# Optimization experiments

Hardware: AMD Instinct MI355X
Metric: run time of the kernel (lower is better)

The kernel has to match this reference:

```python
import jax, jax.numpy as jnp
import numpy as np

B, S, D, DIM = 8, 4096, 1024, 512  # batch, src nodes, dst nodes, feature dim


def setup_inputs() -> dict:
    key = jax.random.key(0)
    k1, k2, k3, k4, k5 = jax.random.split(key, 5)
    scale = 1.0 / np.sqrt(DIM)
    return {
        "src_val": jax.random.normal(k1, (B, S, DIM), dtype=jnp.float32),
        "src_state": jax.random.normal(k2, (B, S), dtype=jnp.float32),
        "dst_val": jax.random.normal(k3, (B, D, DIM), dtype=jnp.float32),
        "W_route": jax.random.normal(k4, (DIM, DIM), dtype=jnp.float32) * scale,
        "W_val": jax.random.normal(k5, (DIM, DIM), dtype=jnp.float32) * scale,
    }


def reference(src_val, src_state, dst_val, W_route, W_val):
    # Pairwise route logits: bilinear bipartite attention, [B, S, D]
    inv_sqrt_d = 1.0 / jnp.sqrt(jnp.asarray(src_val.shape[-1], src_val.dtype))
    q = jnp.einsum("bsd,de->bse", src_val, W_route)
    logits = jnp.einsum("bse,bke->bsk", q, dst_val) * inv_sqrt_d
    # route compression: softmax over dst nodes (dim=-1)
    routes = jax.nn.softmax(logits, axis=-1)
    # projections
    projected_val = jnp.einsum("bsd,de->bse", src_val, W_val)  # [B, S, DIM]
    projected_state = src_state                                 # identity state proj, [B, S]
    sender_strength = jax.nn.softplus(src_state)                # [B, S]
    # weighted routing + accumulation
    weighted_routes = routes * sender_strength[..., None]       # [B, S, D]
    delta_state = jnp.einsum("bsk,bs->bk", weighted_routes, projected_state)   # [B, D]
    delta_val = jnp.einsum("bsk,bsd->bkd", weighted_routes, projected_val)     # [B, D, DIM]
    return delta_state, delta_val
```

## Files before the change

### kernel.cpp

```cpp
#include <hip/hip_runtime.h>
#include <hip/hip_fp16.h>

#define B_   8
#define S_   4096
#define DD_  1024
#define DIM_ 512
#define SCALE 0.044194173824159216f

typedef __bf16 bf16x8 __attribute__((ext_vector_type(8)));
typedef float  floatx4 __attribute__((ext_vector_type(4)));

__device__ inline unsigned short f2bf(float f) {
    union { float f; unsigned int u; } v; v.f = f;
    unsigned int r = v.u + 0x7fffu + ((v.u >> 16) & 1u);
    return (unsigned short)(r >> 16);
}
__device__ inline float bf2f(unsigned short h) {
    union { unsigned int u; float f; } v; v.u = ((unsigned int)h) << 16;
    return v.f;
}
__device__ inline uint4 cvt8(const float* __restrict__ g) {
    float4 f0 = *(const float4*)g;
    float4 f1 = *(const float4*)(g + 4);
    unsigned short tmp[8] = {f2bf(f0.x), f2bf(f0.y), f2bf(f0.z), f2bf(f0.w),
                             f2bf(f1.x), f2bf(f1.y), f2bf(f1.z), f2bf(f1.w)};
    return *(const uint4*)tmp;
}
__device__ inline void async16(unsigned short* lds, const unsigned short* g) {
    __builtin_amdgcn_global_load_lds(
        (const __attribute__((address_space(1))) void*)g,
        (__attribute__((address_space(3))) void*)lds, 16, 0, 0);
}

template <int AF32, int BF32>
__device__ inline void mainloop(unsigned short* As, unsigned short* Bs,
                                const void* Ap, size_t lda,
                                const void* Bp, size_t ldb,
                                int kIters, floatx4 (&acc)[4][4]) {
    const int t = threadIdx.x, lane = t & 63, wave = t >> 6;
    const int rA = t >> 2, cA = (t & 3) * 8;
    const int mrow = (wave >> 1) * 64, ncol = (wave & 1) * 64;
    const int fr = lane & 15, fk = (lane >> 4) * 8;

    const unsigned short* gA16 = nullptr; const float* gA32 = nullptr;
    const unsigned short* gB16 = nullptr; const float* gB32 = nullptr;
    if (AF32) gA32 = (const float*)Ap + (size_t)rA * lda + cA;
    else      gA16 = (const unsigned short*)Ap + (size_t)rA * lda + cA;
    if (BF32) gB32 = (const float*)Bp + (size_t)rA * ldb + cA;
    else      gB16 = (const unsigned short*)Bp + (size_t)rA * ldb + cA;

    unsigned short* ldsA = As + wave * 512;
    unsigned short* ldsB = Bs + wave * 512;

    for (int kt = 0; kt < kIters; ++kt) {
        if (AF32) {
            *(uint4*)&As[t * 8]        = cvt8(gA32);
            *(uint4*)&As[2048 + t * 8] = cvt8(gA32 + 64 * lda);
            gA32 += 32;
        } else {
            async16(ldsA,        gA16);
            async16(ldsA + 2048, gA16 + 64 * lda);
            gA16 += 32;
        }
        if (BF32) {
            *(uint4*)&Bs[t * 8]        = cvt8(gB32);
            *(uint4*)&Bs[2048 + t * 8] = cvt8(gB32 + 64 * ldb);
            gB32 += 32;
        } else {
            async16(ldsB,        gB16);
            async16(ldsB + 2048, gB16 + 64 * ldb);
            gB16 += 32;
        }
        __syncthreads();
        bf16x8 af[4], bfr[4];
#pragma unroll
        for (int i = 0; i < 4; ++i)
            af[i] = *(const bf16x8*)&As[(mrow + i * 16 + fr) * 32 + fk];
#pragma unroll
        for (int j = 0; j < 4; ++j)
            bfr[j] = *(const bf16x8*)&Bs[(ncol + j * 16 + fr) * 32 + fk];
#pragma unroll
        for (int i = 0; i < 4; ++i)
#pragma unroll
            for (int j = 0; j < 4; ++j)
                acc[i][j] = __builtin_amdgcn_mfma_f32_16x16x32_bf16(af[i], bfr[j],
                                                                    acc[i][j], 0, 0, 0);
        __syncthreads();
    }
}

#define EPILOGUE_COORDS                                     \
    const int lane = threadIdx.x & 63, wave = threadIdx.x >> 6; \
    const int mrow = (wave >> 1) * 64, ncol = (wave & 1) * 64;  \
    const int col = lane & 15, q = lane >> 4;

#define ACC_INIT                                            \
    floatx4 acc[4][4];                                      \
    _Pragma("unroll") for (int i = 0; i < 4; ++i)           \
        _Pragma("unroll") for (int j = 0; j < 4; ++j)       \
            acc[i][j] = (floatx4){0.f, 0.f, 0.f, 0.f};

__global__ __launch_bounds__(256) void k_prep(const float* __restrict__ src,
                                              unsigned short* __restrict__ srcb,
                                              const float* __restrict__ dst,
                                              unsigned short* __restrict__ dstb) {
    const int t = threadIdx.x;
    if (blockIdx.x < 8192) {
        const size_t idx = ((size_t)blockIdx.x * 256 + t) * 8;
        *(uint4*)&srcb[idx] = cvt8(src + idx);
    } else {
        const size_t idx = ((size_t)(blockIdx.x - 8192) * 256 + t) * 8;
        *(uint4*)&dstb[idx] = cvt8(dst + idx);
    }
}

__global__ __launch_bounds__(256) void k_dstWr(const unsigned short* __restrict__ dstb,
                                               const float* __restrict__ Wr,
                                               unsigned short* __restrict__ DW) {
    __shared__ unsigned short As[128 * 32];
    __shared__ unsigned short Bs[128 * 32];
    const int n0 = blockIdx.x * 128, m0 = blockIdx.y * 128;
    ACC_INIT
    mainloop<0, 1>(As, Bs, dstb + (size_t)m0 * DIM_, DIM_,
                   Wr + (size_t)n0 * DIM_, DIM_, DIM_ / 32, acc);
    EPILOGUE_COORDS
#pragma unroll
    for (int i = 0; i < 4; ++i)
#pragma unroll
        for (int j = 0; j < 4; ++j)
#pragma unroll
            for (int r = 0; r < 4; ++r)
                DW[(size_t)(m0 + mrow + i * 16 + q * 4 + r) * DIM_ +
                   n0 + ncol + j * 16 + col] = f2bf(acc[i][j][r] * SCALE);
}

__global__ __launch_bounds__(256) void k_logitsT(const unsigned short* __restrict__ DW,
                                                 const unsigned short* __restrict__ srcb,
                                                 unsigned short* __restrict__ LTb,
                                                 float* __restrict__ Lpart) {
    __shared__ unsigned short As[128 * 32];
    __shared__ unsigned short Bs[128 * 32];
    __shared__ float csum[8][128];
    const int n = blockIdx.x;
    const int b = n & 7;
    const int rem = n >> 3;
    const int xs = rem >> 3;
    const int yd = rem & 7;
    const int n0 = xs * 128, m0 = yd * 128;
    ACC_INIT
    mainloop<0, 0>(As, Bs,
                   DW + (size_t)b * DD_ * DIM_ + (size_t)m0 * DIM_, DIM_,
                   srcb + (size_t)b * S_ * DIM_ + (size_t)n0 * DIM_, DIM_,
                   DIM_ / 32, acc);
    EPILOGUE_COORDS
    unsigned short* LT = LTb + (size_t)b * DD_ * S_;
    float psum[4] = {0.f, 0.f, 0.f, 0.f};
#pragma unroll
    for (int i = 0; i < 4; ++i)
#pragma unroll
        for (int j = 0; j < 4; ++j)
#pragma unroll
            for (int r = 0; r < 4; ++r) {
                float e = __expf(acc[i][j][r]);
                LT[(size_t)(m0 + mrow + i * 16 + q * 4 + r) * S_ +
                   n0 + ncol + j * 16 + col] = f2bf(e);
                psum[j] += e;
            }
    const int slice = (wave >> 1) * 4 + q;
#pragma unroll
    for (int j = 0; j < 4; ++j) csum[slice][ncol + j * 16 + col] = psum[j];
    __syncthreads();
    const int t = threadIdx.x;
    if (t < 128) {
        float v = 0.f;
#pragma unroll
        for (int k = 0; k < 8; ++k) v += csum[k][t];
        Lpart[((size_t)b * 8 + yd) * S_ + n0 + t] = v;
    }
}

__global__ __launch_bounds__(256) void k_finalize(const float* __restrict__ state,
                                                  const float* __restrict__ Lpart,
                                                  float* __restrict__ scale) {
    const int i = blockIdx.x * 256 + threadIdx.x;
    const int b = i >> 12, s = i & (S_ - 1);
    float d = 0.f;
#pragma unroll
    for (int k = 0; k < 8; ++k) d += Lpart[((size_t)b * 8 + k) * S_ + s];
    const float st = state[i];
    const float sp = (st > 15.f) ? st : log1pf(__expf(st));
    scale[i] = sp / d;
}

__global__ __launch_bounds__(256) void k_srcT(const unsigned short* __restrict__ srcb,
                                              const float* __restrict__ scale,
                                              unsigned short* __restrict__ srcST) {
    __shared__ unsigned short Ts[64 * 65];
    const int s0 = blockIdx.x * 64, d0 = blockIdx.y * 64, b = blockIdx.z;
    const int t = threadIdx.x;
    {
        const int r = t >> 2, c0 = (t & 3) * 16;
        const unsigned short* g =
            srcb + (size_t)b * S_ * DIM_ + (size_t)(s0 + r) * DIM_ + d0 + c0;
        uint4 v0 = *(const uint4*)g;
        uint4 v1 = *(const uint4*)(g + 8);
        const unsigned short* e0 = (const unsigned short*)&v0;
        const unsigned short* e1 = (const unsigned short*)&v1;
        const float sc = scale[(size_t)b * S_ + s0 + r];
#pragma unroll
        for (int i = 0; i < 8; ++i) {
            Ts[r * 65 + c0 + i]     = f2bf(bf2f(e0[i]) * sc);
            Ts[r * 65 + c0 + 8 + i] = f2bf(bf2f(e1[i]) * sc);
        }
    }
    __syncthreads();
    {
        const int rr = t >> 2, c0 = (t & 3) * 16;
        unsigned short tmp[16];
#pragma unroll
        for (int j = 0; j < 16; ++j) tmp[j] = Ts[(c0 + j) * 65 + rr];
        unsigned short* o =
            srcST + (size_t)b * DIM_ * S_ + (size_t)(d0 + rr) * S_ + s0 + c0;
        *(uint4*)o = *(const uint4*)tmp;
        *(uint4*)(o + 8) = *(const uint4*)(tmp + 8);
    }
}

__global__ __launch_bounds__(256) void k_dstate(const unsigned short* __restrict__ LT,
                                                const float* __restrict__ state,
                                                const float* __restrict__ scale,
                                                float* __restrict__ out) {
    const int b = blockIdx.y;
    const int dd = blockIdx.x * 4 + (threadIdx.x >> 6);
    const int lane = threadIdx.x & 63;
    const unsigned short* row = LT + (size_t)b * DD_ * S_ + (size_t)dd * S_;
    const float* st = state + (size_t)b * S_;
    const float* sc = scale + (size_t)b * S_;

    float acc = 0.f;
#pragma unroll
    for (int it = 0; it < S_ / 512; ++it) {
        const int s = it * 512 + lane * 8;
        uint4 v = *(const uint4*)(row + s);
        const unsigned short* e = (const unsigned short*)&v;
        float4 f0 = *(const float4*)(st + s);
        float4 f1 = *(const float4*)(st + s + 4);
        float4 c0 = *(const float4*)(sc + s);
        float4 c1 = *(const float4*)(sc + s + 4);
        acc += bf2f(e[0]) * f0.x * c0.x + bf2f(e[1]) * f0.y * c0.y +
               bf2f(e[2]) * f0.z * c0.z + bf2f(e[3]) * f0.w * c0.w +
               bf2f(e[4]) * f1.x * c1.x + bf2f(e[5]) * f1.y * c1.y +
               bf2f(e[6]) * f1.z * c1.z + bf2f(e[7]) * f1.w * c1.w;
    }
#pragma unroll
    for (int off = 32; off; off >>= 1) acc += __shfl_down(acc, off);
    if (lane == 0) out[(size_t)b * DD_ + dd] = acc;
}

__global__ __launch_bounds__(256) void k_dU(const unsigned short* __restrict__ LTb,
                                            const unsigned short* __restrict__ srcST,
                                            __half* __restrict__ Pp) {
    __shared__ unsigned short As[128 * 32];
    __shared__ unsigned short Bs[128 * 32];
    const int n = blockIdx.x;
    const int z = (n & 7) + 8 * (n >> 8);
    const int rem = (n >> 3) & 31;
    const int xe = rem >> 3;
    const int yd = rem & 7;
    const int b = z >> 2, ks = z & 3;
    const int n0 = xe * 128, m0 = yd * 128;
    ACC_INIT
    mainloop<0, 0>(As, Bs,
                   LTb + (size_t)b * DD_ * S_ + (size_t)m0 * S_ + ks * 1024, S_,
                   srcST + (size_t)b * DIM_ * S_ + (size_t)n0 * S_ + ks * 1024, S_,
                   1024 / 32, acc);
    EPILOGUE_COORDS
    __half* O = Pp + (size_t)ks * B_ * DD_ * DIM_ + (size_t)b * DD_ * DIM_;
#pragma unroll
    for (int i = 0; i < 4; ++i)
#pragma unroll
        for (int j = 0; j < 4; ++j)
#pragma unroll
            for (int r = 0; r < 4; ++r)
                O[(size_t)(m0 + mrow + i * 16 + q * 4 + r) * DIM_ +
                  n0 + ncol + j * 16 + col] = __float2half(acc[i][j][r]);
}

__global__ __launch_bounds__(256) void k_reduceU(const __half* __restrict__ Pp,
                                                 unsigned short* __restrict__ U,
                                                 const float* __restrict__ Wv,
                                                 unsigned short* __restrict__ WvT) {
    __shared__ float Ts[64 * 68];
    const int t = threadIdx.x;
    if (blockIdx.x < 2048) {
        const size_t idx = ((size_t)blockIdx.x * 256 + t) * 8;
        const size_t n = (size_t)B_ * DD_ * DIM_;
        float o[8] = {0.f, 0.f, 0.f, 0.f, 0.f, 0.f, 0.f, 0.f};
#pragma unroll
        for (int ks = 0; ks < 4; ++ks) {
            uint4 v = *(const uint4*)(Pp + (size_t)ks * n + idx);
            const __half* h = (const __half*)&v;
#pragma unroll
            for (int j = 0; j < 8; ++j) o[j] += __half2float(h[j]);
        }
        unsigned short tmp[8];
#pragma unroll
        for (int j = 0; j < 8; ++j) tmp[j] = f2bf(o[j]);
        *(uint4*)&U[idx] = *(const uint4*)tmp;
        return;
    }
    const int n2 = blockIdx.x - 2048;
    const int d0 = (n2 & 7) * 64, e0 = (n2 >> 3) * 64;
    {
        const int r = t >> 2, c0 = (t & 3) * 16;
        const float* g = Wv + (size_t)(d0 + r) * DIM_ + e0 + c0;
#pragma unroll
        for (int i = 0; i < 4; ++i)
            *(float4*)&Ts[r * 68 + c0 + i * 4] = *(const float4*)(g + i * 4);
    }
    __syncthreads();
    {
        const int rr = t >> 2, c0 = (t & 3) * 16;
        unsigned short tmp[16];
#pragma unroll
        for (int j = 0; j < 16; ++j) tmp[j] = f2bf(Ts[(c0 + j) * 68 + rr]);
        unsigned short* o = WvT + (size_t)(e0 + rr) * DIM_ + d0 + c0;
        *(uint4*)o = *(const uint4*)tmp;
        *(uint4*)(o + 8) = *(const uint4*)(tmp + 8);
    }
}

__global__ __launch_bounds__(256) void k_dvalW(const unsigned short* __restrict__ U,
                                               const unsigned short* __restrict__ WvT,
                                               float* __restrict__ d_val) {
    __shared__ unsigned short As[128 * 32];
    __shared__ unsigned short Bs[128 * 32];
    const int n0 = blockIdx.x * 128, m0 = blockIdx.y * 128;
    ACC_INIT
    mainloop<0, 0>(As, Bs, U + (size_t)m0 * DIM_, DIM_,
                   WvT + (size_t)n0 * DIM_, DIM_, DIM_ / 32, acc);
    EPILOGUE_COORDS
#pragma unroll
    for (int i = 0; i < 4; ++i)
#pragma unroll
        for (int j = 0; j < 4; ++j)
#pragma unroll
            for (int r = 0; r < 4; ++r)
                d_val[(size_t)(m0 + mrow + i * 16 + q * 4 + r) * DIM_ +
                      n0 + ncol + j * 16 + col] = acc[i][j][r];
}

extern "C" void kernel_launch(void* const* d_in, const int* in_sizes, int n_in,
                              void* d_out, int out_size, void* d_ws, size_t ws_size,
                              hipStream_t stream) {
    const float* src   = (const float*)d_in[0];
    const float* state = (const float*)d_in[1];
    const float* dst   = (const float*)d_in[2];
    const float* Wr    = (const float*)d_in[3];
    const float* Wv    = (const float*)d_in[4];

    unsigned short* srcb = (unsigned short*)d_ws;
    __half* Pp = (__half*)d_ws;
    unsigned short* LT = srcb + (size_t)B_ * S_ * DIM_;
    unsigned short* U  = LT;
    unsigned short* WvT = U + (size_t)B_ * DD_ * DIM_;
    unsigned short* C = LT + (size_t)B_ * DD_ * S_;
    unsigned short* dstb = C;
    unsigned short* DW = dstb + (size_t)B_ * DD_ * DIM_;
    float* Lpart = (float*)(DW + (size_t)B_ * DD_ * DIM_);
    unsigned short* srcST = C;

    float* d_state = (float*)d_out;
    float* d_val   = (float*)d_out + B_ * DD_;
    float* scale   = d_val;

    k_prep<<<dim3(8192 + 2048), 256, 0, stream>>>(src, srcb, dst, dstb);
    k_dstWr<<<dim3(DIM_ / 128, (B_ * DD_) / 128), 256, 0, stream>>>(dstb, Wr, DW);
    k_logitsT<<<dim3(2048), 256, 0, stream>>>(DW, srcb, LT, Lpart);
    k_finalize<<<dim3((B_ * S_) / 256), 256, 0, stream>>>(state, Lpart, scale);
    k_dstate<<<dim3(DD_ / 4, B_), 256, 0, stream>>>(LT, state, scale, d_state);
    k_srcT<<<dim3(S_ / 64, DIM_ / 64, B_), 256, 0, stream>>>(srcb, scale, srcST);
    k_dU<<<dim3(1024), 256, 0, stream>>>(LT, srcST, Pp);
    k_reduceU<<<dim3(2048 + 64), 256, 0, stream>>>(Pp, U, Wv, WvT);
    k_dvalW<<<dim3(DIM_ / 128, (B_ * DD_) / 128), 256, 0, stream>>>(U, WvT, d_val);
}
```

Baseline: 298.0 us.

## Fold delta_state into dU GEMM and stage epilogue stores through LDS

Removes the separate k_dstate kernel, which re-read the whole exp-logit matrix LT. Instead, the xe==0 blocks of k_dU compute a dot product of the LT tile already in LDS with precomputed scale*state weights, and k_reduceU sums the per-split partials. The epilogues of k_logitsT and k_dU now go through an LDS staging buffer, replacing scattered 2-byte global stores with coalesced 16-byte row writes. This costs extra LDS, more barriers, and some load imbalance on the folding blocks.

Measured after the change: 314.9 us. 5.7% more time.

```diff
diff --git a/kernel.cpp b/kernel.cpp
--- a/kernel.cpp
+++ b/kernel.cpp
@@ -18,6 +18,10 @@
 __device__ inline float bf2f(unsigned short h) {
     union { unsigned int u; float f; } v; v.u = ((unsigned int)h) << 16;
     return v.f;
+}
+__device__ inline unsigned short f2h(float f) {
+    __half h = __float2half(f);
+    union { __half h; unsigned short u; } v; v.h = h; return v.u;
 }
 __device__ inline uint4 cvt8(const float* __restrict__ g) {
     float4 f0 = *(const float4*)g;
@@ -140,6 +144,7 @@
                                                  float* __restrict__ Lpart) {
     __shared__ unsigned short As[128 * 32];
     __shared__ unsigned short Bs[128 * 32];
+    __shared__ __align__(16) unsigned short Rep[64 * 136];
     __shared__ float csum[8][128];
     const int n = blockIdx.x;
     const int b = n & 7;
@@ -153,24 +158,55 @@
                    srcb + (size_t)b * S_ * DIM_ + (size_t)n0 * DIM_, DIM_,
                    DIM_ / 32, acc);
     EPILOGUE_COORDS
+    const int t = threadIdx.x;
     unsigned short* LT = LTb + (size_t)b * DD_ * S_;
     float psum[4] = {0.f, 0.f, 0.f, 0.f};
-#pragma unroll
-    for (int i = 0; i < 4; ++i)
-#pragma unroll
-        for (int j = 0; j < 4; ++j)
-#pragma unroll
-            for (int r = 0; r < 4; ++r) {
-                float e = __expf(acc[i][j][r]);
-                LT[(size_t)(m0 + mrow + i * 16 + q * 4 + r) * S_ +
-                   n0 + ncol + j * 16 + col] = f2bf(e);
-                psum[j] += e;
-            }
-    const int slice = (wave >> 1) * 4 + q;
+    const int myp = wave >> 1;
+    const int rrow = t >> 2, rcg = (t & 3) * 32;
+
+    if (myp == 0) {
+#pragma unroll
+        for (int i = 0; i < 4; ++i)
+#pragma unroll
+            for (int j = 0; j < 4; ++j)
+#pragma unroll
+                for (int r = 0; r < 4; ++r) {
+                    float e = __expf(acc[i][j][r]);
+                    Rep[(i * 16 + q * 4 + r) * 136 + ncol + j * 16 + col] = f2bf(e);
+                    psum[j] += e;
+                }
+    }
+    __syncthreads();
+    {
+        unsigned short* o = LT + (size_t)(m0 + rrow) * S_ + n0 + rcg;
+        const unsigned short* rp = &Rep[rrow * 136 + rcg];
+#pragma unroll
+        for (int k = 0; k < 4; ++k) *(uint4*)(o + k * 8) = *(const uint4*)(rp + k * 8);
+    }
+    __syncthreads();
+    if (myp == 1) {
+#pragma unroll
+        for (int i = 0; i < 4; ++i)
+#pragma unroll
+            for (int j = 0; j < 4; ++j)
+#pragma unroll
+                for (int r = 0; r < 4; ++r) {
+                    float e = __expf(acc[i][j][r]);
+                    Rep[(i * 16 + q * 4 + r) * 136 + ncol + j * 16 + col] = f2bf(e);
+                    psum[j] += e;
+                }
+    }
+    __syncthreads();
+    {
+        unsigned short* o = LT + (size_t)(m0 + 64 + rrow) * S_ + n0 + rcg;
+        const unsigned short* rp = &Rep[rrow * 136 + rcg];
+#pragma unroll
+        for (int k = 0; k < 4; ++k) *(uint4*)(o + k * 8) = *(const uint4*)(rp + k * 8);
+    }
+    const int slice = myp * 4 + q;
 #pragma unroll
     for (int j = 0; j < 4; ++j) csum[slice][ncol + j * 16 + col] = psum[j];
     __syncthreads();
-    const int t = threadIdx.x;
     if (t < 128) {
         float v = 0.f;
 #pragma unroll
@@ -181,7 +217,8 @@
 
 __global__ __launch_bounds__(256) void k_finalize(const float* __restrict__ state,
                                                   const float* __restrict__ Lpart,
-                                                  float* __restrict__ scale) {
+                                                  float* __restrict__ scale,
+                                                  float* __restrict__ wst) {
     const int i = blockIdx.x * 256 + threadIdx.x;
     const int b = i >> 12, s = i & (S_ - 1);
     float d = 0.f;
@@ -189,7 +226,9 @@
     for (int k = 0; k < 8; ++k) d += Lpart[((size_t)b * 8 + k) * S_ + s];
     const float st = state[i];
     const float sp = (st > 15.f) ? st : log1pf(__expf(st));
-    scale[i] = sp / d;
+    const float sc = sp / d;
+    scale[i] = sc;
+    wst[i] = sc * st;
 }
 
 __global__ __launch_bounds__(256) void k_srcT(const unsigned short* __restrict__ srcb,
@@ -226,42 +265,15 @@
     }
 }
 
-__global__ __launch_bounds__(256) void k_dstate(const unsigned short* __restrict__ LT,
-                                                const float* __restrict__ state,
-                                                const float* __restrict__ scale,
-                                                float* __restrict__ out) {
-    const int b = blockIdx.y;
-    const int dd = blockIdx.x * 4 + (threadIdx.x >> 6);
-    const int lane = threadIdx.x & 63;
-    const unsigned short* row = LT + (size_t)b * DD_ * S_ + (size_t)dd * S_;
-    const float* st = state + (size_t)b * S_;
-    const float* sc = scale + (size_t)b * S_;
-
-    float acc = 0.f;
-#pragma unroll
-    for (int it = 0; it < S_ / 512; ++it) {
-        const int s = it * 512 + lane * 8;
-        uint4 v = *(const uint4*)(row + s);
-        const unsigned short* e = (const unsigned short*)&v;
-        float4 f0 = *(const float4*)(st + s);
-        float4 f1 = *(const float4*)(st + s + 4);
-        float4 c0 = *(const float4*)(sc + s);
-        float4 c1 = *(const float4*)(sc + s + 4);
-        acc += bf2f(e[0]) * f0.x * c0.x + bf2f(e[1]) * f0.y * c0.y +
-               bf2f(e[2]) * f0.z * c0.z + bf2f(e[3]) * f0.w * c0.w +
-               bf2f(e[4]) * f1.x * c1.x + bf2f(e[5]) * f1.y * c1.y +
-               bf2f(e[6]) * f1.z * c1.z + bf2f(e[7]) * f1.w * c1.w;
-    }
-#pragma unroll
-    for (int off = 32; off; off >>= 1) acc += __shfl_down(acc, off);
-    if (lane == 0) out[(size_t)b * DD_ + dd] = acc;
-}
-
 __global__ __launch_bounds__(256) void k_dU(const unsigned short* __restrict__ LTb,
                                             const unsigned short* __restrict__ srcST,
-                                            __half* __restrict__ Pp) {
+                                            const float* __restrict__ wst,
+                                            __half* __restrict__ Pp,
+                                            float* __restrict__ Dp) {
     __shared__ unsigned short As[128 * 32];
     __shared__ unsigned short Bs[128 * 32];
+    __shared__ __align__(16) unsigned short Rep[64 * 136];
+    __shared__ float wlds[1024];
     const int n = blockIdx.x;
     const int z = (n & 7) + 8 * (n >> 8);
     const int rem = (n >> 3) & 31;
@@ -269,27 +281,110 @@
     const int yd = rem & 7;
     const int b = z >> 2, ks = z & 3;
     const int n0 = xe * 128, m0 = yd * 128;
+    const int t = threadIdx.x, lane = t & 63, wave = t >> 6;
+    const int rA = t >> 2, cA = (t & 3) * 8;
+    const int mrow = (wave >> 1) * 64, ncol = (wave & 1) * 64;
+    const int fr = lane & 15, fk = (lane >> 4) * 8;
+    const bool dofold = (xe == 0);
+    if (dofold)
+        *(float4*)&wlds[t * 4] =
+            *(const float4*)(wst + (size_t)b * S_ + ks * 1024 + t * 4);
+
     ACC_INIT
-    mainloop<0, 0>(As, Bs,
-                   LTb + (size_t)b * DD_ * S_ + (size_t)m0 * S_ + ks * 1024, S_,
-                   srcST + (size_t)b * DIM_ * S_ + (size_t)n0 * S_ + ks * 1024, S_,
-                   1024 / 32, acc);
-    EPILOGUE_COORDS
-    __half* O = Pp + (size_t)ks * B_ * DD_ * DIM_ + (size_t)b * DD_ * DIM_;
-#pragma unroll
-    for (int i = 0; i < 4; ++i)
+    const unsigned short* gA =
+        LTb + (size_t)b * DD_ * S_ + (size_t)(m0 + rA) * S_ + ks * 1024 + cA;
+    const unsigned short* gB =
+        srcST + (size_t)b * DIM_ * S_ + (size_t)(n0 + rA) * S_ + ks * 1024 + cA;
+    unsigned short* ldsA = As + wave * 512;
+    unsigned short* ldsB = Bs + wave * 512;
+    float dacc = 0.f;
+    const int drow = t >> 1, dkh = (t & 1) * 16;
+
+    for (int kt = 0; kt < 32; ++kt) {
+        async16(ldsA,        gA);
+        async16(ldsA + 2048, gA + 64 * S_);
+        async16(ldsB,        gB);
+        async16(ldsB + 2048, gB + 64 * S_);
+        gA += 32; gB += 32;
+        __syncthreads();
+        bf16x8 af[4], bfr[4];
+#pragma unroll
+        for (int i = 0; i < 4; ++i)
+            af[i] = *(const bf16x8*)&As[(mrow + i * 16 + fr) * 32 + fk];
 #pragma unroll
         for (int j = 0; j < 4; ++j)
-#pragma unroll
-            for (int r = 0; r < 4; ++r)
-                O[(size_t)(m0 + mrow + i * 16 + q * 4 + r) * DIM_ +
-                  n0 + ncol + j * 16 + col] = __float2half(acc[i][j][r]);
+            bfr[j] = *(const bf16x8*)&Bs[(ncol + j * 16 + fr) * 32 + fk];
+#pragma unroll
+        for (int i = 0; i < 4; ++i)
+#pragma unroll
+            for (int j = 0; j < 4; ++j)
+                acc[i][j] = __builtin_amdgcn_mfma_f32_16x16x32_bf16(af[i], bfr[j],
+                                                                    acc[i][j], 0, 0, 0);
+        if (dofold) {
+            bf16x8 v0 = *(const bf16x8*)&As[drow * 32 + dkh];
+            bf16x8 v1 = *(const bf16x8*)&As[drow * 32 + dkh + 8];
+            const float* wp = &wlds[kt * 32 + dkh];
+            float p = 0.f;
+#pragma unroll
+            for (int jj = 0; jj < 8; ++jj)
+                p += (float)v0[jj] * wp[jj] + (float)v1[jj] * wp[jj + 8];
+            dacc += p;
+        }
+        __syncthreads();
+    }
+    if (dofold) {
+        dacc += __shfl_xor(dacc, 1);
+        if (!(t & 1)) Dp[((size_t)(b * 4 + ks)) * 1024 + m0 + drow] = dacc;
+    }
+
+    unsigned short* O = (unsigned short*)Pp + (size_t)ks * B_ * DD_ * DIM_ +
+                        (size_t)b * DD_ * DIM_;
+    const int col = fr, q = lane >> 4;
+    const int myp = wave >> 1;
+    const int rrow = t >> 2, rcg = (t & 3) * 32;
+    if (myp == 0) {
+#pragma unroll
+        for (int i = 0; i < 4; ++i)
+#pragma unroll
+            for (int j = 0; j < 4; ++j)
+#pragma unroll
+                for (int r = 0; r < 4; ++r)
+                    Rep[(i * 16 + q * 4 + r) * 136 + ncol + j * 16 + col] =
+                        f2h(acc[i][j][r]);
+    }
+    __syncthreads();
+    {
+        unsigned short* o = O + (size_t)(m0 + rrow) * DIM_ + n0 + rcg;
+        const unsigned short* rp = &Rep[rrow * 136 + rcg];
+#pragma unroll
+        for (int k = 0; k < 4; ++k) *(uint4*)(o + k * 8) = *(const uint4*)(rp + k * 8);
+    }
+    __syncthreads();
+    if (myp == 1) {
+#pragma unroll
+        for (int i = 0; i < 4; ++i)
+#pragma unroll
+            for (int j = 0; j < 4; ++j)
+#pragma unroll
+                for (int r = 0; r < 4; ++r)
+                    Rep[(i * 16 + q * 4 + r) * 136 + ncol + j * 16 + col] =
+                        f2h(acc[i][j][r]);
+    }
+    __syncthreads();
+    {
+        unsigned short* o = O + (size_t)(m0 + 64 + rrow) * DIM_ + n0 + rcg;
+        const unsigned short* rp = &Rep[rrow * 136 + rcg];
+#pragma unroll
+        for (int k = 0; k < 4; ++k) *(uint4*)(o + k * 8) = *(const uint4*)(rp + k * 8);
+    }
 }
 
 __global__ __launch_bounds__(256) void k_reduceU(const __half* __restrict__ Pp,
                                                  unsigned short* __restrict__ U,
                                                  const float* __restrict__ Wv,
-                                                 unsigned short* __restrict__ WvT) {
+                                                 unsigned short* __restrict__ WvT,
+                                                 const float* __restrict__ Dp,
+                                                 float* __restrict__ d_state) {
     __shared__ float Ts[64 * 68];
     const int t = threadIdx.x;
     if (blockIdx.x < 2048) {
@@ -307,6 +402,15 @@
 #pragma unroll
         for (int j = 0; j < 8; ++j) tmp[j] = f2bf(o[j]);
         *(uint4*)&U[idx] = *(const uint4*)tmp;
+        return;
+    }
+    if (blockIdx.x >= 2112) {
+        const int flat = (blockIdx.x - 2112) * 256 + t;
+        const int bb = flat >> 10, dd = flat & 1023;
+        float v = 0.f;
+#pragma unroll
+        for (int ks = 0; ks < 4; ++ks) v += Dp[((size_t)(bb * 4 + ks)) * 1024 + dd];
+        d_state[(size_t)bb * DD_ + dd] = v;
         return;
     }
     const int n2 = blockIdx.x - 2048;
@@ -373,14 +477,15 @@
     float* d_state = (float*)d_out;
     float* d_val   = (float*)d_out + B_ * DD_;
     float* scale   = d_val;
+    float* wst     = d_val + (size_t)B_ * S_;
+    float* Dp      = d_val + 2 * (size_t)B_ * S_;
 
     k_prep<<<dim3(8192 + 2048), 256, 0, stream>>>(src, srcb, dst, dstb);
     k_dstWr<<<dim3(DIM_ / 128, (B_ * DD_) / 128), 256, 0, stream>>>(dstb, Wr, DW);
     k_logitsT<<<dim3(2048), 256, 0, stream>>>(DW, srcb, LT, Lpart);
-    k_finalize<<<dim3((B_ * S_) / 256), 256, 0, stream>>>(state, Lpart, scale);
-    k_dstate<<<dim3(DD_ / 4, B_), 256, 0, stream>>>(LT, state, scale, d_state);
+    k_finalize<<<dim3((B_ * S_) / 256), 256, 0, stream>>>(state, Lpart, scale, wst);
     k_srcT<<<dim3(S_ / 64, DIM_ / 64, B_), 256, 0, stream>>>(srcb, scale, srcST);
-    k_dU<<<dim3(1024), 256, 0, stream>>>(LT, srcST, Pp);
-    k_reduceU<<<dim3(2048 + 64), 256, 0, stream>>>(Pp, U, Wv, WvT);
+    k_dU<<<dim3(1024), 256, 0, stream>>>(LT, srcST, wst, Pp, Dp);
+    k_reduceU<<<dim3(2048 + 64 + 32), 256, 0, stream>>>(Pp, U, Wv, WvT, Dp, d_state);
     k_dvalW<<<dim3(DIM_ / 128, (B_ * DD_) / 128), 256, 0, stream>>>(U, WvT, d_val);
 }
```
